# Kernel tuning notes

Hardware: AMD Instinct MI355X
Metric: run time of the kernel (lower is better)

The kernel has to match this reference:

```python
import jax, jax.numpy as jnp
import numpy as np

N, E, H, C, NG = 50000, 800000, 4, 64, 32
HC = H * C  # 256


def setup_inputs() -> dict:
    key = jax.random.key(0)
    ks = jax.random.split(key, 32)
    f32 = jnp.float32
    def rn(k, shape, s=0.1):
        return jax.random.normal(k, shape, dtype=f32) * s
    inp = {}
    inp['x'] = jax.random.normal(ks[0], (N, 4), dtype=f32)
    inp['edge_index'] = jax.random.randint(ks[1], (2, E), 0, N, dtype=jnp.int32)
    inp['edge_attr'] = jax.random.normal(ks[2], (E, 1), dtype=f32)
    inp['batch'] = jnp.sort(jax.random.randint(ks[3], (N,), 0, NG, dtype=jnp.int32))
    # encoder
    inp['enc_w'] = rn(ks[4], (4, 64)); inp['enc_b'] = rn(ks[5], (64,))
    # GATv2 layer 1: in 64 -> H*C (lin_l source, lin_r target, lin_edge, att, bias)
    inp['g1_wl'] = rn(ks[6], (64, HC)); inp['g1_bl'] = rn(ks[7], (HC,))
    inp['g1_wr'] = rn(ks[8], (64, HC)); inp['g1_br'] = rn(ks[9], (HC,))
    inp['g1_we'] = rn(ks[10], (1, HC))
    inp['g1_att'] = rn(ks[11], (H, C))
    inp['g1_bias'] = rn(ks[12], (HC,))
    # GATv2 layer 2: in 256 -> H*C
    inp['g2_wl'] = rn(ks[13], (HC, HC)); inp['g2_bl'] = rn(ks[14], (HC,))
    inp['g2_wr'] = rn(ks[15], (HC, HC)); inp['g2_br'] = rn(ks[16], (HC,))
    inp['g2_we'] = rn(ks[17], (1, HC))
    inp['g2_att'] = rn(ks[18], (H, C))
    inp['g2_bias'] = rn(ks[19], (HC,))
    # post MLP: 256 -> 128 (LayerNorm, ReLU) -> 64 (ReLU)
    inp['p1_w'] = rn(ks[20], (HC, 128)); inp['p1_b'] = rn(ks[21], (128,))
    inp['ln_g'] = jnp.ones((128,), dtype=f32); inp['ln_b'] = jnp.zeros((128,), dtype=f32)
    inp['p2_w'] = rn(ks[22], (128, 64)); inp['p2_b'] = rn(ks[23], (64,))
    return inp


def _gatv2_layer(x, src, dst, eattr, wl, bl, wr, br, we, att, bias):
    # PyG GATv2Conv: alpha_e = att . leaky_relu(lin_l(x_src) + lin_r(x_dst) + lin_edge(e))
    n = x.shape[0]
    xl = (x @ wl + bl).reshape(n, H, C)   # source-side messages
    xr = (x @ wr + br).reshape(n, H, C)   # target-side
    e = (eattr @ we).reshape(-1, H, C)
    m = jax.nn.leaky_relu(xl[src] + xr[dst] + e, 0.2)        # [E',H,C]
    alpha = jnp.einsum('ehc,hc->eh', m, att)                  # [E',H]
    amax = jax.lax.stop_gradient(jax.ops.segment_max(alpha, dst, num_segments=n))
    ex = jnp.exp(alpha - amax[dst])
    den = jax.ops.segment_sum(ex, dst, num_segments=n)
    a = ex / den[dst]                                          # softmax per dst node
    out = jax.ops.segment_sum(a[:, :, None] * xl[src], dst, num_segments=n)
    return out.reshape(n, HC) + bias


def reference(x, edge_index, edge_attr, batch, enc_w, enc_b,
              g1_wl, g1_bl, g1_wr, g1_br, g1_we, g1_att, g1_bias,
              g2_wl, g2_bl, g2_wr, g2_br, g2_we, g2_att, g2_bias,
              p1_w, p1_b, ln_g, ln_b, p2_w, p2_b):
    n = x.shape[0]
    src0, dst0 = edge_index[0], edge_index[1]
    # PyG default add_self_loops=True with fill_value='mean' for edge_attr
    deg = jnp.maximum(jax.ops.segment_sum(jnp.ones_like(edge_attr[:, 0]), dst0, num_segments=n), 1.0)
    loop_attr = jax.ops.segment_sum(edge_attr, dst0, num_segments=n) / deg[:, None]
    idx = jnp.arange(n, dtype=src0.dtype)
    src = jnp.concatenate([src0, idx]); dst = jnp.concatenate([dst0, idx])
    eattr = jnp.concatenate([edge_attr, loop_attr], axis=0)
    h = jax.nn.relu(x @ enc_w + enc_b)
    h = jax.nn.relu(_gatv2_layer(h, src, dst, eattr, g1_wl, g1_bl, g1_wr, g1_br, g1_we, g1_att, g1_bias))
    h = jax.nn.relu(_gatv2_layer(h, src, dst, eattr, g2_wl, g2_bl, g2_wr, g2_br, g2_we, g2_att, g2_bias))
    # global mean pool over graphs
    cnt = jnp.maximum(jax.ops.segment_sum(jnp.ones((n,), h.dtype), batch, num_segments=NG), 1.0)
    g = jax.ops.segment_sum(h, batch, num_segments=NG) / cnt[:, None]
    # post MLP (dropout is identity in eval)
    z = g @ p1_w + p1_b
    mu = jnp.mean(z, axis=-1, keepdims=True)
    var = jnp.mean((z - mu) ** 2, axis=-1, keepdims=True)
    z = (z - mu) / jnp.sqrt(var + 1e-5) * ln_g + ln_b
    z = jax.nn.relu(z)
    z = jax.nn.relu(z @ p2_w + p2_b)
    return z
```

## Files before the change

kernel.cpp:

```cpp
#include <hip/hip_runtime.h>

#define CDIV(a,b) (((a)+(b)-1)/(b))

typedef __bf16 bf16_t;
typedef unsigned char u8;
typedef bf16_t bf16x8 __attribute__((ext_vector_type(8)));
typedef float floatx4 __attribute__((ext_vector_type(4)));
typedef float floatx2 __attribute__((ext_vector_type(2)));

__device__ __forceinline__ int sigma2(int p) {
    int tile = p >> 7, hh = (p >> 6) & 1, m = (p >> 2) & 15, c = p & 3;
    return tile * 128 + (hh * 4 + c) * 16 + m;
}

__device__ __forceinline__ unsigned pack4_fp8(float a, float b, float c, float d) {
    int v = __builtin_amdgcn_cvt_pk_fp8_f32(a, b, 0, false);
    v = __builtin_amdgcn_cvt_pk_fp8_f32(c, d, v, true);
    return (unsigned)v;
}

template<bool HI>
__device__ __forceinline__ floatx2 cvtf8(unsigned v) {
    return __builtin_amdgcn_cvt_pk_f32_fp8(v, HI);
}

__global__ void k_deg(const int* __restrict__ ei, int* __restrict__ deg, int E) {
    int e = blockIdx.x * 256 + threadIdx.x;
    if (e >= E) return;
    atomicAdd(&deg[ei[E + e]], 1);
}

__global__ void k_scanA(const int* __restrict__ deg, int* __restrict__ part, int n) {
    __shared__ int sh[256];
    int t = threadIdx.x;
    int i = blockIdx.x * 256 + t;
    int v = (i < n) ? deg[i] + 1 : 0;
    sh[t] = v;
    __syncthreads();
    for (int d = 128; d > 0; d >>= 1) { if (t < d) sh[t] += sh[t + d]; __syncthreads(); }
    if (t == 0) part[blockIdx.x] = sh[0];
}
__global__ void k_scanB(int* __restrict__ part, int nb) {
    __shared__ int sh[256];
    int t = threadIdx.x;
    int v = (t < nb) ? part[t] : 0;
    sh[t] = v;
    __syncthreads();
    for (int d = 1; d < 256; d <<= 1) {
        int u = (t >= d) ? sh[t - d] : 0;
        __syncthreads();
        sh[t] += u;
        __syncthreads();
    }
    if (t < nb) part[t] = sh[t] - v;
}
__global__ void k_scanC(const int* __restrict__ deg, const int* __restrict__ part,
                        int* __restrict__ off, int n) {
    __shared__ int sh[256];
    int t = threadIdx.x;
    int i = blockIdx.x * 256 + t;
    int v = (i < n) ? deg[i] + 1 : 0;
    sh[t] = v;
    __syncthreads();
    for (int d = 1; d < 256; d <<= 1) {
        int u = (t >= d) ? sh[t - d] : 0;
        __syncthreads();
        sh[t] += u;
        __syncthreads();
    }
    int excl = part[blockIdx.x] + sh[t] - v;
    if (i < n) off[i] = excl;
    if (i == n - 1) off[n] = excl + v;
}

__global__ void k_fill(const int* __restrict__ ei, const float* __restrict__ ea,
                       const int* __restrict__ off, int* __restrict__ cursor,
                       int2* __restrict__ csr, int E) {
    int e = blockIdx.x * 256 + threadIdx.x;
    if (e >= E) return;
    int s = ei[e], d = ei[E + e];
    int pos = off[d] + atomicAdd(&cursor[d], 1);
    csr[pos] = make_int2(s, __float_as_int(ea[e]));
}

__global__ void k_selfloop(const int* __restrict__ off, int2* __restrict__ csr, int n) {
    int i = blockIdx.x * 256 + threadIdx.x;
    if (i >= n) return;
    int p0 = off[i], p1 = off[i + 1] - 1;
    float s = 0.0f;
    for (int p = p0; p < p1; ++p) s += __int_as_float(csr[p].y);
    float la = s / fmaxf((float)(p1 - p0), 1.0f);
    csr[p1] = make_int2(i, __float_as_int(la));
}

__global__ void k_wcast2(const float* __restrict__ Wl, const float* __restrict__ Wr,
                         const float* __restrict__ bl, const float* __restrict__ br,
                         bf16_t* __restrict__ Wt, float* __restrict__ bias2,
                         int K, int kshift, int permK,
                         const float* __restrict__ we, const float* __restrict__ att,
                         const float* __restrict__ cb,
                         float* __restrict__ wep, float* __restrict__ attp,
                         float* __restrict__ cbp) {
    int idx = blockIdx.x * 256 + threadIdx.x;
    if (idx < 512) bias2[idx] = (idx < 256) ? bl[idx] : br[idx - 256];
    if (idx < 256) {
        int sg = sigma2(idx);
        wep[idx] = we[sg]; attp[idx] = att[sg]; cbp[idx] = cb[sg];
    }
    if (idx >= 512 * K) return;
    int nn = idx >> kshift, k = idx & (K - 1);
    int ks = permK ? sigma2(k) : k;
    float v = (nn < 256) ? Wl[ks * 256 + nn] : Wr[ks * 256 + (nn - 256)];
    Wt[idx] = (bf16_t)v;
}

__global__ __launch_bounds__(256) void k_gemm1_fused(
        const float* __restrict__ x, const float* __restrict__ encw,
        const float* __restrict__ encb, const bf16_t* __restrict__ Wt,
        const float* __restrict__ bias2, u8* __restrict__ XL,
        u8* __restrict__ XR, int nrows) {
    __shared__ bf16_t As[128 * 32];
    __shared__ bf16_t Bs[128 * 32];
    int tid = threadIdx.x;
    int w = tid >> 6, lane = tid & 63;
    int quad = lane >> 4, m = lane & 15;
    int row0 = blockIdx.x * 128;
    int ct0 = blockIdx.y * 2;
    bf16x8 afr[2][2];
    floatx4 acc[2][8];

    for (int ctile = ct0; ctile < ct0 + 2; ++ctile) {
        int n0 = ctile * 128;
#pragma unroll
        for (int rt = 0; rt < 2; ++rt)
#pragma unroll
            for (int ct = 0; ct < 8; ++ct)
                acc[rt][ct] = (floatx4){0.f, 0.f, 0.f, 0.f};
        for (int k0c = 0; k0c < 2; ++k0c) {
            __syncthreads();
            if (ctile == ct0) {
#pragma unroll
                for (int i = 0; i < 2; ++i) {
                    int c = tid + i * 256;
                    int r = c >> 2, kc = c & 3;
                    int sw = (kc + (r >> 1)) & 3;
                    int gr = row0 + r; if (gr >= nrows) gr = nrows - 1;
                    float4 xv = ((const float4*)x)[gr];
                    bf16x8 v;
#pragma unroll
                    for (int kk = 0; kk < 8; ++kk) {
                        int k = k0c * 32 + kc * 8 + kk;
                        float s = encb[k];
                        s = fmaf(xv.x, encw[k], s);
                        s = fmaf(xv.y, encw[64 + k], s);
                        s = fmaf(xv.z, encw[128 + k], s);
                        s = fmaf(xv.w, encw[192 + k], s);
                        v[kk] = (bf16_t)fmaxf(s, 0.0f);
                    }
                    *(bf16x8*)&As[r * 32 + sw * 8] = v;
                }
            }
#pragma unroll
            for (int i = 0; i < 2; ++i) {
                int c = tid + i * 256;
                int r = c >> 2, kc = c & 3;
                int sw = (kc + (r >> 1)) & 3;
                bf16x8 v = *(const bf16x8*)&Wt[(size_t)(n0 + r) * 64 + k0c * 32 + kc * 8];
                *(bf16x8*)&Bs[r * 32 + sw * 8] = v;
            }
            __syncthreads();
            if (ctile == ct0) {
#pragma unroll
                for (int rt = 0; rt < 2; ++rt) {
                    int ar = w * 32 + rt * 16 + m;
                    afr[k0c][rt] = *(bf16x8*)&As[ar * 32 + (((quad + (ar >> 1)) & 3) * 8)];
                }
            }
            bf16x8 bfr[8];
#pragma unroll
            for (int ct = 0; ct < 8; ++ct) {
                int br = ct * 16 + m;
                bfr[ct] = *(bf16x8*)&Bs[br * 32 + (((quad + (br >> 1)) & 3) * 8)];
            }
#pragma unroll
            for (int ct = 0; ct < 8; ++ct) {
                acc[0][ct] = __builtin_amdgcn_mfma_f32_16x16x32_bf16(afr[k0c][0], bfr[ct], acc[0][ct], 0, 0, 0);
                acc[1][ct] = __builtin_amdgcn_mfma_f32_16x16x32_bf16(afr[k0c][1], bfr[ct], acc[1][ct], 0, 0, 0);
            }
        }
        int tile = ctile & 1;
        u8* dst = (ctile < 2) ? XL : XR;
        float bv[8];
#pragma unroll
        for (int ct = 0; ct < 8; ++ct) bv[ct] = bias2[n0 + ct * 16 + m];
#pragma unroll
        for (int rt = 0; rt < 2; ++rt) {
#pragma unroll
            for (int i = 0; i < 4; ++i) {
                int row = row0 + w * 32 + rt * 16 + quad * 4 + i;
                if (row < nrows) {
                    unsigned w0 = pack4_fp8(acc[rt][0][i] + bv[0], acc[rt][1][i] + bv[1],
                                            acc[rt][2][i] + bv[2], acc[rt][3][i] + bv[3]);
                    unsigned w1 = pack4_fp8(acc[rt][4][i] + bv[4], acc[rt][5][i] + bv[5],
                                            acc[rt][6][i] + bv[6], acc[rt][7][i] + bv[7]);
                    *(unsigned*)&dst[(size_t)row * 256 + tile * 128 + m * 4] = w0;
                    *(unsigned*)&dst[(size_t)row * 256 + tile * 128 + 64 + m * 4] = w1;
                }
            }
        }
    }
}

__global__ __launch_bounds__(256) void k_gemm2(
        const bf16_t* __restrict__ Hb, const bf16_t* __restrict__ Wt,
        const float* __restrict__ bias2, u8* __restrict__ XL,
        u8* __restrict__ XR, int nrows) {
    const int K = 256;
    __shared__ bf16_t As[128 * 32];
    __shared__ bf16_t Bs[128 * 32];
    int tid = threadIdx.x;
    int w = tid >> 6, lane = tid & 63;
    int quad = lane >> 4, m = lane & 15;
    int row0 = blockIdx.x * 128;
    int ct0 = blockIdx.y * 2;
    bf16x8 afr[8][2];
    floatx4 acc[2][8];

    for (int ctile = ct0; ctile < ct0 + 2; ++ctile) {
        int n0 = ctile * 128;
#pragma unroll
        for (int rt = 0; rt < 2; ++rt)
#pragma unroll
            for (int ct = 0; ct < 8; ++ct)
                acc[rt][ct] = (floatx4){0.f, 0.f, 0.f, 0.f};
        for (int k0c = 0; k0c < 8; ++k0c) {
            __syncthreads();
            if (ctile == ct0) {
#pragma unroll
                for (int i = 0; i < 2; ++i) {
                    int c = tid + i * 256;
                    int r = c >> 2, kc = c & 3;
                    int sw = (kc + (r >> 1)) & 3;
                    int gr = row0 + r; if (gr >= nrows) gr = nrows - 1;
                    bf16x8 v = *(const bf16x8*)&Hb[(size_t)gr * K + k0c * 32 + kc * 8];
                    *(bf16x8*)&As[r * 32 + sw * 8] = v;
                }
            }
#pragma unroll
            for (int i = 0; i < 2; ++i) {
                int c = tid + i * 256;
                int r = c >> 2, kc = c & 3;
                int sw = (kc + (r >> 1)) & 3;
                bf16x8 v = *(const bf16x8*)&Wt[(size_t)(n0 + r) * K + k0c * 32 + kc * 8];
                *(bf16x8*)&Bs[r * 32 + sw * 8] = v;
            }
            __syncthreads();
            if (ctile == ct0) {
#pragma unroll
                for (int rt = 0; rt < 2; ++rt) {
                    int ar = w * 32 + rt * 16 + m;
                    afr[k0c][rt] = *(bf16x8*)&As[ar * 32 + (((quad + (ar >> 1)) & 3) * 8)];
                }
            }
            bf16x8 bfr[8];
#pragma unroll
            for (int ct = 0; ct < 8; ++ct) {
                int br = ct * 16 + m;
                bfr[ct] = *(bf16x8*)&Bs[br * 32 + (((quad + (br >> 1)) & 3) * 8)];
            }
#pragma unroll
            for (int ct = 0; ct < 8; ++ct) {
                acc[0][ct] = __builtin_amdgcn_mfma_f32_16x16x32_bf16(afr[k0c][0], bfr[ct], acc[0][ct], 0, 0, 0);
                acc[1][ct] = __builtin_amdgcn_mfma_f32_16x16x32_bf16(afr[k0c][1], bfr[ct], acc[1][ct], 0, 0, 0);
            }
        }
        int tile = ctile & 1;
        u8* dst = (ctile < 2) ? XL : XR;
        float bv[8];
#pragma unroll
        for (int ct = 0; ct < 8; ++ct) bv[ct] = bias2[n0 + ct * 16 + m];
#pragma unroll
        for (int rt = 0; rt < 2; ++rt) {
#pragma unroll
            for (int i = 0; i < 4; ++i) {
                int row = row0 + w * 32 + rt * 16 + quad * 4 + i;
                if (row < nrows) {
                    unsigned w0 = pack4_fp8(acc[rt][0][i] + bv[0], acc[rt][1][i] + bv[1],
                                            acc[rt][2][i] + bv[2], acc[rt][3][i] + bv[3]);
                    unsigned w1 = pack4_fp8(acc[rt][4][i] + bv[4], acc[rt][5][i] + bv[5],
                                            acc[rt][6][i] + bv[6], acc[rt][7][i] + bv[7]);
                    *(unsigned*)&dst[(size_t)row * 256 + tile * 128 + m * 4] = w0;
                    *(unsigned*)&dst[(size_t)row * 256 + tile * 128 + 64 + m * 4] = w1;
                }
            }
        }
    }
}

__device__ __forceinline__ void pair_step(
        int p, int p1, int half, int loff,
        const int2* __restrict__ csr, const u8* __restrict__ XL,
        floatx2 xr01, floatx2 xr23, floatx2 xr45, floatx2 xr67,
        floatx2 wv01, floatx2 wv23, floatx2 wv45, floatx2 wv67,
        floatx2 av01, floatx2 av23, floatx2 av45, floatx2 av67,
        float& s, floatx2& a01, floatx2& a23, floatx2& a45, floatx2& a67) {
    int idx = p + half;
    bool valid = idx < p1;
    int idc = valid ? idx : p1 - 1;
    int2 ed = csr[idc];
    int src = ed.x;
    float eav = __int_as_float(ed.y);
    uint2 u = *(const uint2*)(XL + (size_t)src * 256 + loff);
    floatx2 x01 = cvtf8<false>(u.x);
    floatx2 x23 = cvtf8<true>(u.x);
    floatx2 x45 = cvtf8<false>(u.y);
    floatx2 x67 = cvtf8<true>(u.y);
    floatx2 t01 = x01 + xr01 + eav * wv01;
    floatx2 t23 = x23 + xr23 + eav * wv23;
    floatx2 t45 = x45 + xr45 + eav * wv45;
    floatx2 t67 = x67 + xr67 + eav * wv67;
    t01 = __builtin_elementwise_max(t01, 0.2f * t01);
    t23 = __builtin_elementwise_max(t23, 0.2f * t23);
    t45 = __builtin_elementwise_max(t45, 0.2f * t45);
    t67 = __builtin_elementwise_max(t67, 0.2f * t67);
    floatx2 d = t01 * av01 + t23 * av23 + t45 * av45 + t67 * av67;
    float al = d.x + d.y;
    al += __shfl_xor(al, 1);
    al += __shfl_xor(al, 2);
    al += __shfl_xor(al, 4);
    float wg = valid ? exp2f(al) : 0.0f;
    s += wg;
    a01 += wg * x01; a23 += wg * x23; a45 += wg * x45; a67 += wg * x67;
}

__global__ void k_conv(
                       const u8* __restrict__ XL, const u8* __restrict__ XR,
                       const float* __restrict__ wep, const float* __restrict__ attp,
                       const int2* __restrict__ csr,
                       const int* __restrict__ off, const float* __restrict__ cbp,
                       bf16_t* __restrict__ outb, int n) {
    int wid = (blockIdx.x * 256 + threadIdx.x) >> 6;
    int lane = threadIdx.x & 63;
    if (wid >= n) return;
    int l = lane & 31, half = lane >> 5;
    int loff = l * 8;
    uint2 ur = *(const uint2*)(XR + (size_t)wid * 256 + loff);
    floatx2 xr01 = cvtf8<false>(ur.x);
    floatx2 xr23 = cvtf8<true>(ur.x);
    floatx2 xr45 = cvtf8<false>(ur.y);
    floatx2 xr67 = cvtf8<true>(ur.y);
    float4 wa = ((const float4*)wep)[2 * l], wb = ((const float4*)wep)[2 * l + 1];
    float4 aa = ((const float4*)attp)[2 * l], ab = ((const float4*)attp)[2 * l + 1];
    floatx2 wv01 = {wa.x, wa.y}, wv23 = {wa.z, wa.w};
    floatx2 wv45 = {wb.x, wb.y}, wv67 = {wb.z, wb.w};
    const float LOG2E = 1.44269504f;
    floatx2 av01 = {aa.x * LOG2E, aa.y * LOG2E}, av23 = {aa.z * LOG2E, aa.w * LOG2E};
    floatx2 av45 = {ab.x * LOG2E, ab.y * LOG2E}, av67 = {ab.z * LOG2E, ab.w * LOG2E};
    int p0 = off[wid], p1 = off[wid + 1];
    float s = 0.f;
    floatx2 a01 = {0.f, 0.f}, a23 = {0.f, 0.f}, a45 = {0.f, 0.f}, a67 = {0.f, 0.f};
    int p = p0;
    for (; p + 4 <= p1; p += 4) {
        pair_step(p,     p1, half, loff, csr, XL, xr01, xr23, xr45, xr67,
                  wv01, wv23, wv45, wv67, av01, av23, av45, av67, s, a01, a23, a45, a67);
        pair_step(p + 2, p1, half, loff, csr, XL, xr01, xr23, xr45, xr67,
                  wv01, wv23, wv45, wv67, av01, av23, av45, av67, s, a01, a23, a45, a67);
    }
    for (; p < p1; p += 2)
        pair_step(p,     p1, half, loff, csr, XL, xr01, xr23, xr45, xr67,
                  wv01, wv23, wv45, wv67, av01, av23, av45, av67, s, a01, a23, a45, a67);
    s += __shfl_xor(s, 32);
    a01.x += __shfl_xor(a01.x, 32); a01.y += __shfl_xor(a01.y, 32);
    a23.x += __shfl_xor(a23.x, 32); a23.y += __shfl_xor(a23.y, 32);
    a45.x += __shfl_xor(a45.x, 32); a45.y += __shfl_xor(a45.y, 32);
    a67.x += __shfl_xor(a67.x, 32); a67.y += __shfl_xor(a67.y, 32);
    if (half == 0) {
        float inv = 1.0f / s;
        float4 ba = ((const float4*)cbp)[2 * l], bb = ((const float4*)cbp)[2 * l + 1];
        bf16x8 ob;
        ob[0] = (bf16_t)fmaxf(fmaf(a01.x, inv, ba.x), 0.f);
        ob[1] = (bf16_t)fmaxf(fmaf(a01.y, inv, ba.y), 0.f);
        ob[2] = (bf16_t)fmaxf(fmaf(a23.x, inv, ba.z), 0.f);
        ob[3] = (bf16_t)fmaxf(fmaf(a23.y, inv, ba.w), 0.f);
        ob[4] = (bf16_t)fmaxf(fmaf(a45.x, inv, bb.x), 0.f);
        ob[5] = (bf16_t)fmaxf(fmaf(a45.y, inv, bb.y), 0.f);
        ob[6] = (bf16_t)fmaxf(fmaf(a67.x, inv, bb.z), 0.f);
        ob[7] = (bf16_t)fmaxf(fmaf(a67.y, inv, bb.w), 0.f);
        *(bf16x8*)&outb[(size_t)wid * 256 + l * 8] = ob;
    }
}

__global__ void k_pool(const bf16_t* __restrict__ h, const int* __restrict__ batch,
                       float* __restrict__ gsum, float* __restrict__ gcnt, int n) {
    int j = threadIdx.x;
    int start = blockIdx.x * 32;
    if (start >= n) return;
    int end = start + 32; if (end > n) end = n;
    int cur = batch[start];
    float acc = 0.0f, cnt = 0.0f;
    for (int i = start; i < end; ++i) {
        int g = batch[i];
        if (g != cur) {
            atomicAdd(&gsum[cur * 256 + j], acc);
            if (j == 0) atomicAdd(&gcnt[cur], cnt);
            acc = 0.0f; cnt = 0.0f; cur = g;
        }
        acc += (float)h[(size_t)i * 256 + j];
        cnt += 1.0f;
    }
    atomicAdd(&gsum[cur * 256 + j], acc);
    if (j == 0) atomicAdd(&gcnt[cur], cnt);
}

__global__ void k_mlp(const float* __restrict__ gsum, const float* __restrict__ gcnt,
                      const float* __restrict__ p1w, const float* __restrict__ p1b,
                      const float* __restrict__ lng, const float* __restrict__ lnb,
                      const float* __restrict__ p2w, const float* __restrict__ p2b,
                      float* __restrict__ out) {
    int g = blockIdx.x;
    int t = threadIdx.x;
    __shared__ float gv[256];
    __shared__ float z[128];
    __shared__ float red[128];
    float invc = 1.0f / fmaxf(gcnt[g], 1.0f);
    gv[sigma2(t)]       = gsum[g * 256 + t] * invc;
    gv[sigma2(t + 128)] = gsum[g * 256 + 128 + t] * invc;
    __syncthreads();
    float z1 = p1b[t];
    for (int k = 0; k < 256; ++k) z1 = fmaf(gv[k], p1w[k * 128 + t], z1);
    red[t] = z1;
    __syncthreads();
    for (int d = 64; d > 0; d >>= 1) { if (t < d) red[t] += red[t + d]; __syncthreads(); }
    float mu = red[0] * (1.0f / 128.0f);
    __syncthreads();
    float dz = z1 - mu;
    red[t] = dz * dz;
    __syncthreads();
    for (int d = 64; d > 0; d >>= 1) { if (t < d) red[t] += red[t + d]; __syncthreads(); }
    float var = red[0] * (1.0f / 128.0f);
    float zn = dz * rsqrtf(var + 1e-5f) * lng[t] + lnb[t];
    z[t] = fmaxf(zn, 0.0f);
    __syncthreads();
    if (t < 64) {
        float o = p2b[t];
        for (int k = 0; k < 128; ++k) o = fmaf(z[k], p2w[k * 64 + t], o);
        out[g * 64 + t] = fmaxf(o, 0.0f);
    }
}

extern "C" void kernel_launch(void* const* d_in, const int* in_sizes, int n_in,
                              void* d_out, int out_size, void* d_ws, size_t ws_size,
                              hipStream_t stream) {
    const float* x      = (const float*)d_in[0];
    const int*   ei     = (const int*)d_in[1];
    const float* ea     = (const float*)d_in[2];
    const int*   batch  = (const int*)d_in[3];
    const float* enc_w  = (const float*)d_in[4];
    const float* enc_b  = (const float*)d_in[5];
    const float* g1_wl  = (const float*)d_in[6];
    const float* g1_bl  = (const float*)d_in[7];
    const float* g1_wr  = (const float*)d_in[8];
    const float* g1_br  = (const float*)d_in[9];
    const float* g1_we  = (const float*)d_in[10];
    const float* g1_att = (const float*)d_in[11];
    const float* g1_bias= (const float*)d_in[12];
    const float* g2_wl  = (const float*)d_in[13];
    const float* g2_bl  = (const float*)d_in[14];
    const float* g2_wr  = (const float*)d_in[15];
    const float* g2_br  = (const float*)d_in[16];
    const float* g2_we  = (const float*)d_in[17];
    const float* g2_att = (const float*)d_in[18];
    const float* g2_bias= (const float*)d_in[19];
    const float* p1_w   = (const float*)d_in[20];
    const float* p1_b   = (const float*)d_in[21];
    const float* ln_g   = (const float*)d_in[22];
    const float* ln_b   = (const float*)d_in[23];
    const float* p2_w   = (const float*)d_in[24];
    const float* p2_b   = (const float*)d_in[25];
    float* out = (float*)d_out;

    const int N  = in_sizes[3];
    const int E  = in_sizes[1] / 2;
    const int EE = E + N;
    const int NB = CDIV(N, 256);

    u8*     XL  = (u8*)d_ws;
    u8*     XR  = XL + (size_t)N * 256;
    bf16_t* Hb  = (bf16_t*)(XR + (size_t)N * 256);
    bf16_t* Wt  = Hb + (size_t)N * 256;
    int2*  csr  = (int2*)(Wt + 512 * 256);
    float* gsum  = (float*)(csr + EE);
    float* gcnt  = gsum + 32 * 256;
    int*   deg   = (int*)(gcnt + 32);
    int*   cursor= deg + N;
    float* bias2 = (float*)(cursor + N);
    float* wep   = bias2 + 512;
    float* attp  = wep + 256;
    float* cbp   = attp + 256;
    int*   part  = (int*)(cbp + 256);
    int*   off   = part + 256;

    (void)hipMemsetAsync(gsum, 0, (size_t)(2 * N + 32 * 256 + 32) * sizeof(float), stream);

    k_deg<<<CDIV(E, 256), 256, 0, stream>>>(ei, deg, E);
    k_scanA<<<NB, 256, 0, stream>>>(deg, part, N);
    k_scanB<<<1, 256, 0, stream>>>(part, NB);
    k_scanC<<<NB, 256, 0, stream>>>(deg, part, off, N);
    k_fill<<<CDIV(E, 256), 256, 0, stream>>>(ei, ea, off, cursor, csr, E);
    k_selfloop<<<NB, 256, 0, stream>>>(off, csr, N);

    dim3 ggrid(CDIV(N, 128), 2);

    k_wcast2<<<CDIV(512 * 64, 256), 256, 0, stream>>>(g1_wl, g1_wr, g1_bl, g1_br, Wt, bias2,
                                                      64, 6, 0, g1_we, g1_att, g1_bias,
                                                      wep, attp, cbp);
    k_gemm1_fused<<<ggrid, 256, 0, stream>>>(x, enc_w, enc_b, Wt, bias2, XL, XR, N);
    k_conv<<<CDIV(N, 4), 256, 0, stream>>>(XL, XR, wep, attp, csr, off, cbp, Hb, N);

    k_wcast2<<<CDIV(512 * 256, 256), 256, 0, stream>>>(g2_wl, g2_wr, g2_bl, g2_br, Wt, bias2,
                                                       256, 8, 1, g2_we, g2_att, g2_bias,
                                                       wep, attp, cbp);
    k_gemm2<<<ggrid, 256, 0, stream>>>(Hb, Wt, bias2, XL, XR, N);
    k_conv<<<CDIV(N, 4), 256, 0, stream>>>(XL, XR, wep, attp, csr, off, cbp, Hb, N);

    k_pool<<<CDIV(N, 32), 256, 0, stream>>>(Hb, batch, gsum, gcnt, N);
    k_mlp<<<32, 128, 0, stream>>>(gsum, gcnt, p1_w, p1_b, ln_g, ln_b, p2_w, p2_b, out);
}
```

Baseline: 447.8 us.

## Batch CSR loads per wave and software-pipeline neighbor gathers in GATv2 conv

```diff
diff --git a/kernel.cpp b/kernel.cpp
--- a/kernel.cpp
+++ b/kernel.cpp
@@ -22,6 +22,12 @@
 template<bool HI>
 __device__ __forceinline__ floatx2 cvtf8(unsigned v) {
     return __builtin_amdgcn_cvt_pk_f32_fp8(v, HI);
+}
+
+template<int CTRL>
+__device__ __forceinline__ float dpp_add(float x) {
+    int v = __builtin_amdgcn_update_dpp(0, __float_as_int(x), CTRL, 0xf, 0xf, true);
+    return x + __int_as_float(v);
 }
 
 __global__ void k_deg(const int* __restrict__ ei, int* __restrict__ deg, int E) {
@@ -295,42 +301,6 @@
             }
         }
     }
-}
-
-__device__ __forceinline__ void pair_step(
-        int p, int p1, int half, int loff,
-        const int2* __restrict__ csr, const u8* __restrict__ XL,
-        floatx2 xr01, floatx2 xr23, floatx2 xr45, floatx2 xr67,
-        floatx2 wv01, floatx2 wv23, floatx2 wv45, floatx2 wv67,
-        floatx2 av01, floatx2 av23, floatx2 av45, floatx2 av67,
-        float& s, floatx2& a01, floatx2& a23, floatx2& a45, floatx2& a67) {
-    int idx = p + half;
-    bool valid = idx < p1;
-    int idc = valid ? idx : p1 - 1;
-    int2 ed = csr[idc];
-    int src = ed.x;
-    float eav = __int_as_float(ed.y);
-    uint2 u = *(const uint2*)(XL + (size_t)src * 256 + loff);
-    floatx2 x01 = cvtf8<false>(u.x);
-    floatx2 x23 = cvtf8<true>(u.x);
-    floatx2 x45 = cvtf8<false>(u.y);
-    floatx2 x67 = cvtf8<true>(u.y);
-    floatx2 t01 = x01 + xr01 + eav * wv01;
-    floatx2 t23 = x23 + xr23 + eav * wv23;
-    floatx2 t45 = x45 + xr45 + eav * wv45;
-    floatx2 t67 = x67 + xr67 + eav * wv67;
-    t01 = __builtin_elementwise_max(t01, 0.2f * t01);
-    t23 = __builtin_elementwise_max(t23, 0.2f * t23);
-    t45 = __builtin_elementwise_max(t45, 0.2f * t45);
-    t67 = __builtin_elementwise_max(t67, 0.2f * t67);
-    floatx2 d = t01 * av01 + t23 * av23 + t45 * av45 + t67 * av67;
-    float al = d.x + d.y;
-    al += __shfl_xor(al, 1);
-    al += __shfl_xor(al, 2);
-    al += __shfl_xor(al, 4);
-    float wg = valid ? exp2f(al) : 0.0f;
-    s += wg;
-    a01 += wg * x01; a23 += wg * x23; a45 += wg * x45; a67 += wg * x67;
 }
 
 __global__ void k_conv(
@@ -359,16 +329,53 @@
     int p0 = off[wid], p1 = off[wid + 1];
     float s = 0.f;
     floatx2 a01 = {0.f, 0.f}, a23 = {0.f, 0.f}, a45 = {0.f, 0.f}, a67 = {0.f, 0.f};
-    int p = p0;
-    for (; p + 4 <= p1; p += 4) {
-        pair_step(p,     p1, half, loff, csr, XL, xr01, xr23, xr45, xr67,
-                  wv01, wv23, wv45, wv67, av01, av23, av45, av67, s, a01, a23, a45, a67);
-        pair_step(p + 2, p1, half, loff, csr, XL, xr01, xr23, xr45, xr67,
-                  wv01, wv23, wv45, wv67, av01, av23, av45, av67, s, a01, a23, a45, a67);
-    }
-    for (; p < p1; p += 2)
-        pair_step(p,     p1, half, loff, csr, XL, xr01, xr23, xr45, xr67,
-                  wv01, wv23, wv45, wv67, av01, av23, av45, av67, s, a01, a23, a45, a67);
+
+    for (int base = p0; base < p1; base += 64) {
+        int rem = p1 - base;
+        int cnt = (rem < 64) ? rem : 64;
+        int gp = base + lane; if (gp > p1 - 1) gp = p1 - 1;
+        int2 ed = csr[gp];
+
+        auto fetch = [&](int j, uint2& u, float& ev) {
+            int sl = j + half; if (sl >= cnt) sl = cnt - 1;
+            int sx = __shfl(ed.x, sl);
+            ev = __int_as_float(__shfl(ed.y, sl));
+            u = *(const uint2*)(XL + (size_t)sx * 256 + loff);
+        };
+
+        uint2 u0, u1, u2; float e0, e1, e2;
+        fetch(0, u0, e0);
+        fetch(2, u1, e1);
+        fetch(4, u2, e2);
+
+#pragma unroll 3
+        for (int j = 0; j < cnt; j += 2) {
+            uint2 un; float en;
+            fetch(j + 6, un, en);
+            floatx2 x01 = cvtf8<false>(u0.x);
+            floatx2 x23 = cvtf8<true>(u0.x);
+            floatx2 x45 = cvtf8<false>(u0.y);
+            floatx2 x67 = cvtf8<true>(u0.y);
+            floatx2 t01 = x01 + xr01 + e0 * wv01;
+            floatx2 t23 = x23 + xr23 + e0 * wv23;
+            floatx2 t45 = x45 + xr45 + e0 * wv45;
+            floatx2 t67 = x67 + xr67 + e0 * wv67;
+            t01 = __builtin_elementwise_max(t01, 0.2f * t01);
+            t23 = __builtin_elementwise_max(t23, 0.2f * t23);
+            t45 = __builtin_elementwise_max(t45, 0.2f * t45);
+            t67 = __builtin_elementwise_max(t67, 0.2f * t67);
+            floatx2 d = t01 * av01 + t23 * av23 + t45 * av45 + t67 * av67;
+            float al = d.x + d.y;
+            al = dpp_add<0xB1>(al);
+            al = dpp_add<0x4E>(al);
+            al = dpp_add<0x141>(al);
+            float wg = (j + half < cnt) ? exp2f(al) : 0.0f;
+            s += wg;
+            a01 += wg * x01; a23 += wg * x23; a45 += wg * x45; a67 += wg * x67;
+            u0 = u1; e0 = e1; u1 = u2; e1 = e2; u2 = un; e2 = en;
+        }
+    }
+
     s += __shfl_xor(s, 32);
     a01.x += __shfl_xor(a01.x, 32); a01.y += __shfl_xor(a01.y, 32);
     a23.x += __shfl_xor(a23.x, 32); a23.y += __shfl_xor(a23.y, 32);
```

Result: faster. 425.3 us (-5.0%).
